# Optimization experiments

Hardware: AMD Instinct MI355X
Metric: run time of the kernel (lower is better)

Reference implementation:

```python
import jax, jax.numpy as jnp
import numpy as np


def _log_kernel(ks, sigma):
    ax = np.arange(-(ks // 2), ks // 2 + 1, dtype=np.float64)
    xx, yy = np.meshgrid(ax, ax, indexing='ij')
    r2 = xx ** 2 + yy ** 2
    gaussian = np.exp(-r2 / (2 * sigma ** 2))
    laplacian = -1.0 / (np.pi * sigma ** 4) * (1.0 - r2 / (2 * sigma ** 2))
    k = laplacian * gaussian
    k = k / np.sum(np.abs(k))
    return jnp.asarray(k, jnp.float32)


def _hpf_kernel(ks):
    if ks == 3:
        k = np.array([[-1, -1, -1], [-1, 8, -1], [-1, -1, -1]], dtype=np.float32)
    else:  # 5
        k = -np.ones((5, 5), dtype=np.float32)
        k[2, 2] = 24.0
    return jnp.asarray(k)


def _lpf_kernel():
    k = np.array([[1, 2, 1], [2, 4, 2], [1, 2, 1]], dtype=np.float32) / 16.0
    return jnp.asarray(k)


def _gabor_kernel(angle, frequency=0.1, sigma_x=2.0, sigma_y=2.0):
    theta = np.radians(angle)
    x, y = np.meshgrid(np.linspace(-3, 3, 7), np.linspace(-3, 3, 7))
    x_t = x * np.cos(theta) + y * np.sin(theta)
    y_t = -x * np.sin(theta) + y * np.cos(theta)
    g = np.exp(-(x_t ** 2 / sigma_x ** 2 + y_t ** 2 / sigma_y ** 2) / 2.0) * np.cos(2 * np.pi * frequency * x_t)
    g = g / np.sum(np.abs(g))
    return jnp.asarray(g, jnp.float32)


def _dwconv(x, k2d, pad):
    # depthwise conv: same single-channel kernel applied to every channel
    C = x.shape[1]
    kern = jnp.broadcast_to(k2d[None, None], (C, 1) + k2d.shape)  # (C,1,kh,kw)
    return jax.lax.conv_general_dilated(
        x, kern, window_strides=(1, 1), padding=[(pad, pad), (pad, pad)],
        feature_group_count=C, dimension_numbers=('NCHW', 'OIHW', 'NCHW'))


def _squash(z):
    # (tanh(z*0.1)+1)/2
    return (jnp.tanh(z * 0.1) + 1.0) * 0.5


def setup_inputs() -> dict:
    key = jax.random.key(0)
    x = jax.random.normal(key, (16, 3, 512, 512), dtype=jnp.float32)
    return {"x": x, "use_gabor": 1}


def reference(x, use_gabor):
    # 'original'
    original = x
    # 'lpf'
    lpf = _dwconv(x, _lpf_kernel(), pad=1)
    # 'log': multi-scale LoG -> squash -> elementwise max over scales
    log3 = _dwconv(x, _log_kernel(3, 0.8), pad=1)
    log5 = _dwconv(x, _log_kernel(5, 1.0), pad=2)
    log7 = _dwconv(x, _log_kernel(7, 1.4), pad=3)
    log_out = jnp.maximum(jnp.maximum(_squash(log3), _squash(log5)), _squash(log7))
    # 'hpf'
    hpf3 = _dwconv(x, _hpf_kernel(3), pad=1)
    hpf5 = _dwconv(x, _hpf_kernel(5), pad=2)
    hpf_out = jnp.maximum(_squash(hpf3), _squash(hpf5))
    outs = (original, lpf, log_out, hpf_out)
    if use_gabor:
        gab = None
        for angle in (0, 45, 90, 135):
            r = jnp.tanh(_dwconv(x, _gabor_kernel(angle), pad=3) * 0.1)
            gab = r if gab is None else jnp.maximum(gab, r)
        outs = outs + (gab,)
    return outs
```

## Files before the change

kernel.cpp:

```cpp
#include <hip/hip_runtime.h>

#define IMG_H 512
#define IMG_W 512
#define TILE_W 64
#define TILE_H 16
#define LDSW 72
#define LDSH 22
#define TCOLS 72
#define TROWS 16
#define NSLOTA (TROWS * (TCOLS / 4))
#define NTHREADS 256


constexpr double PI_D = 3.141592653589793238462643383279502884;

constexpr double cexp(double x) {
  double term = 1.0, sum = 1.0;
  for (int n = 1; n < 48; ++n) { term *= x / n; sum += term; }
  return sum;
}
constexpr double ccos(double x) {
  double term = 1.0, sum = 1.0;
  for (int n = 1; n < 24; ++n) {
    term *= -x * x / ((2.0 * n - 1.0) * (2.0 * n));
    sum += term;
  }
  return sum;
}
constexpr double csin(double x) {
  double term = x, sum = x;
  for (int n = 1; n < 24; ++n) {
    term *= -x * x / ((2.0 * n) * (2.0 * n + 1.0));
    sum += term;
  }
  return sum;
}
constexpr double cabs_(double x) { return x < 0 ? -x : x; }

constexpr void fill_log(int ks, double sigma, float* out) {
  double buf[49] = {};
  double s = 0.0;
  const int h = ks / 2;
  for (int i = 0; i < ks; ++i) {
    for (int j = 0; j < ks; ++j) {
      const double xi = (double)(i - h);
      const double yj = (double)(j - h);
      const double r2 = xi * xi + yj * yj;
      const double g = cexp(-r2 / (2.0 * sigma * sigma));
      const double lap = -1.0 / (PI_D * sigma * sigma * sigma * sigma) *
                         (1.0 - r2 / (2.0 * sigma * sigma));
      buf[i * ks + j] = lap * g;
      s += cabs_(lap * g);
    }
  }
  for (int k = 0; k < ks * ks; ++k) out[k] = (float)(buf[k] / s);
}

constexpr void fill_log_sep(int ks, double sigma, float* va, float* g, float* wb) {
  const int h = ks / 2;
  double s = 0.0;
  for (int i = 0; i < ks; ++i)
    for (int j = 0; j < ks; ++j) {
      const double xi = (double)(i - h), yj = (double)(j - h);
      const double r2 = xi * xi + yj * yj;
      const double gg = cexp(-r2 / (2.0 * sigma * sigma));
      const double lap = -1.0 / (PI_D * sigma * sigma * sigma * sigma) *
                         (1.0 - r2 / (2.0 * sigma * sigma));
      s += cabs_(lap * gg);
    }
  const double c = 1.0 / (PI_D * sigma * sigma * sigma * sigma);
  for (int i = 0; i < ks; ++i) {
    const double d = (double)(i - h);
    const double gi = cexp(-d * d / (2.0 * sigma * sigma));
    g[i] = (float)gi;
    va[i] = (float)((-c + c * d * d / (2.0 * sigma * sigma)) * gi / s);
    wb[i] = (float)((c * d * d / (2.0 * sigma * sigma)) * gi / s);
  }
}

constexpr double gabor_norm(double ang_deg) {
  const double th = ang_deg * PI_D / 180.0;
  const double ct = ccos(th), st = csin(th);
  double s = 0.0;
  for (int i = 0; i < 7; ++i)
    for (int j = 0; j < 7; ++j) {
      const double xv = (double)(j - 3);
      const double yv = (double)(i - 3);
      const double xt = xv * ct + yv * st;
      const double yt = -xv * st + yv * ct;
      const double g = cexp(-(xt * xt / 4.0 + yt * yt / 4.0) / 2.0) *
                       ccos(2.0 * PI_D * 0.1 * xt);
      s += cabs_(g);
    }
  return s;
}

struct SepTabs {
  float l5_va[5], l5_g[5], l5_wb[5];
  float l7_va[7], l7_g[7], l7_wb[7];
  float v_gb[7], v_gc0[7], v_gca[7], v_gsa[7];
  float h_g0[7], h_g90[7], h_gc[7], h_gs[7];
  float is45, is135;
  float l3_m, l3_e, l3_s;
};

constexpr SepTabs make_sep() {
  SepTabs t{};
  fill_log_sep(5, 1.0, t.l5_va, t.l5_g, t.l5_wb);
  fill_log_sep(7, 1.4, t.l7_va, t.l7_g, t.l7_wb);
  const double s0 = gabor_norm(0.0), s90 = gabor_norm(90.0);
  const double s45 = gabor_norm(45.0), s135 = gabor_norm(135.0);
  const double th45 = 45.0 * PI_D / 180.0;
  const double a45 = 2.0 * PI_D * 0.1 * ccos(th45);
  const double b45 = 2.0 * PI_D * 0.1 * csin(th45);
  const double w0 = 2.0 * PI_D * 0.1;
  for (int k = 0; k < 7; ++k) {
    const double d = (double)(k - 3);
    const double gg = cexp(-d * d / 8.0);
    t.v_gb[k]  = (float)gg;
    t.v_gc0[k] = (float)(gg * ccos(w0 * d));
    t.v_gca[k] = (float)(gg * ccos(b45 * d));
    t.v_gsa[k] = (float)(gg * csin(b45 * d));
    t.h_g0[k]  = (float)(gg * ccos(w0 * d) / s0);
    t.h_g90[k] = (float)(gg / s90);
    t.h_gc[k]  = (float)(gg * ccos(a45 * d));
    t.h_gs[k]  = (float)(gg * csin(a45 * d));
  }
  t.is45 = (float)(1.0 / s45);
  t.is135 = (float)(1.0 / s135);
  float l3[9] = {};
  fill_log(3, 0.8, l3);
  t.l3_m = l3[4]; t.l3_e = l3[1]; t.l3_s = l3[0];
  return t;
}

constexpr SepTabs ST = make_sep();


__device__ __forceinline__ float fast_tanh(float x) {
  float e = __builtin_amdgcn_exp2f(x * 2.8853900817779268f);
  return 1.0f - 2.0f * __builtin_amdgcn_rcpf(e + 1.0f);
}
__device__ __forceinline__ float squash_from(float z) {
  return fmaf(fast_tanh(0.1f * z), 0.5f, 0.5f);
}
__device__ __forceinline__ float4 f4z() { return make_float4(0.f, 0.f, 0.f, 0.f); }
__device__ __forceinline__ float4 f4add(float4 a, float4 b) {
  return make_float4(a.x + b.x, a.y + b.y, a.z + b.z, a.w + b.w);
}
__device__ __forceinline__ float4 f4fma(float a, float4 b, float4 c) {
  return make_float4(fmaf(a, b.x, c.x), fmaf(a, b.y, c.y),
                     fmaf(a, b.z, c.z), fmaf(a, b.w, c.w));
}
__device__ __forceinline__ void loadw12(const float* p, float* w) {
  const float4 a = *(const float4*)(p);
  const float4 b = *(const float4*)(p + 4);
  const float4 c = *(const float4*)(p + 8);
  w[0] = a.x; w[1] = a.y; w[2] = a.z; w[3] = a.w;
  w[4] = b.x; w[5] = b.y; w[6] = b.z; w[7] = b.w;
  w[8] = c.x; w[9] = c.y; w[10] = c.z; w[11] = c.w;
}


__global__ __launch_bounds__(NTHREADS, 5)
void msif_kernel(const float* __restrict__ x, float* __restrict__ out,
                 int planes, int do_gab) {
  __shared__ float tile[LDSH * LDSW];
  __shared__ float T[5][TROWS * TCOLS];

  const int tid = threadIdx.x;
  const int tx = tid & 15;
  const int ty = tid >> 4;
  const int x0 = blockIdx.x * TILE_W;
  const int y0 = blockIdx.y * TILE_H;
  const int plane = blockIdx.z;
  const float* __restrict__ in = x + (size_t)plane * (IMG_H * IMG_W);

  const int gx0 = x0 - 4;
  const int gy0 = y0 - 3;
  for (int k = tid; k < LDSH * (LDSW / 4); k += NTHREADS) {
    int r = k / (LDSW / 4);
    int cc = (k - r * (LDSW / 4)) * 4;
    int gy = gy0 + r;
    int gx = gx0 + cc;
    float4 v = make_float4(0.f, 0.f, 0.f, 0.f);
    if ((unsigned)gy < IMG_H) {
      const float* rowp = in + (size_t)gy * IMG_W;
      if (gx >= 0 && gx + 3 < IMG_W) {
        v = *(const float4*)(rowp + gx);
      } else {
        if ((unsigned)(gx + 0) < IMG_W) v.x = rowp[gx + 0];
        if ((unsigned)(gx + 1) < IMG_W) v.y = rowp[gx + 1];
        if ((unsigned)(gx + 2) < IMG_W) v.z = rowp[gx + 2];
        if ((unsigned)(gx + 3) < IMG_W) v.w = rowp[gx + 3];
      }
    }
    *(float4*)&tile[r * LDSW + cc] = v;
  }
  __syncthreads();

  for (int k = tid; k < NSLOTA; k += NTHREADS) {
    const int r = k / (TCOLS / 4);
    const int c4 = (k - r * (TCOLS / 4)) * 4;
    const float* base = &tile[r * LDSW + c4];
    float4 wv[7];
#pragma unroll
    for (int i = 0; i < 7; ++i) wv[i] = *(const float4*)(base + i * LDSW);

    float4 b5 = f4add(f4add(wv[1], wv[2]), f4add(f4add(wv[3], wv[4]), wv[5]));
    float4 l5a = f4z(), l5g = f4z();
#pragma unroll
    for (int i = 0; i < 5; ++i) {
      l5a = f4fma(ST.l5_va[i], wv[i + 1], l5a);
      l5g = f4fma(ST.l5_g[i],  wv[i + 1], l5g);
    }
    float4 l7a = f4z(), l7g = f4z();
#pragma unroll
    for (int i = 0; i < 7; ++i) {
      l7a = f4fma(ST.l7_va[i], wv[i], l7a);
      l7g = f4fma(ST.l7_g[i],  wv[i], l7g);
    }
    const int o = r * TCOLS + c4;
    *(float4*)&T[0][o] = b5;
    *(float4*)&T[1][o] = l5a;
    *(float4*)&T[2][o] = l5g;
    *(float4*)&T[3][o] = l7a;
    *(float4*)&T[4][o] = l7g;
  }
  __syncthreads();

  const size_t fs = (size_t)planes * (IMG_H * IMG_W);
  const size_t off = (size_t)plane * (IMG_H * IMG_W) +
                     (size_t)(y0 + ty) * IMG_W + (x0 + 4 * tx);
  const int toff = ty * TCOLS + 4 * tx;

  {
    float w[12];
    float l7[4] = {}, l5[4] = {}, box[4];

    loadw12(&T[3][toff], w);
#pragma unroll
    for (int dx = 0; dx < 7; ++dx) {
      const float cc = ST.l7_g[dx];
#pragma unroll
      for (int c = 0; c < 4; ++c) l7[c] = fmaf(w[c + dx + 1], cc, l7[c]);
    }
    loadw12(&T[4][toff], w);
#pragma unroll
    for (int dx = 0; dx < 7; ++dx) {
      const float cc = ST.l7_wb[dx];
#pragma unroll
      for (int c = 0; c < 4; ++c) l7[c] = fmaf(w[c + dx + 1], cc, l7[c]);
    }
    loadw12(&T[1][toff], w);
#pragma unroll
    for (int dx = 0; dx < 5; ++dx) {
      const float cc = ST.l5_g[dx];
#pragma unroll
      for (int c = 0; c < 4; ++c) l5[c] = fmaf(w[c + dx + 2], cc, l5[c]);
    }
    loadw12(&T[2][toff], w);
#pragma unroll
    for (int dx = 0; dx < 5; ++dx) {
      const float cc = ST.l5_wb[dx];
#pragma unroll
      for (int c = 0; c < 4; ++c) l5[c] = fmaf(w[c + dx + 2], cc, l5[c]);
    }
    loadw12(&T[0][toff], w);
#pragma unroll
    for (int c = 0; c < 4; ++c)
      box[c] = ((w[c + 2] + w[c + 3]) + (w[c + 4] + w[c + 5])) + w[c + 6];

    float m[4], e[4], s[4];
    loadw12(&tile[(ty + 2) * LDSW + 4 * tx], w);
#pragma unroll
    for (int c = 0; c < 4; ++c) {
      e[c] = w[c + 4];
      s[c] = w[c + 3] + w[c + 5];
    }
    loadw12(&tile[(ty + 4) * LDSW + 4 * tx], w);
#pragma unroll
    for (int c = 0; c < 4; ++c) {
      e[c] += w[c + 4];
      s[c] += w[c + 3] + w[c + 5];
    }
    loadw12(&tile[(ty + 3) * LDSW + 4 * tx], w);
    *(float4*)(out + off) = make_float4(w[4], w[5], w[6], w[7]);
#pragma unroll
    for (int c = 0; c < 4; ++c) {
      m[c] = w[c + 4];
      e[c] += w[c + 3] + w[c + 5];
    }

    float lp[4], lo[4], ho[4];
#pragma unroll
    for (int c = 0; c < 4; ++c) {
      lp[c] = fmaf(0.25f, m[c], fmaf(0.125f, e[c], 0.0625f * s[c]));
      const float l3v = fmaf(ST.l3_m, m[c], fmaf(ST.l3_e, e[c], ST.l3_s * s[c]));
      const float h3v = fmaf(8.f, m[c], -(e[c] + s[c]));
      const float h5v = fmaf(25.f, m[c], -box[c]);
      lo[c] = squash_from(fmaxf(fmaxf(l3v, l5[c]), l7[c]));
      ho[c] = squash_from(fmaxf(h3v, h5v));
    }
    *(float4*)(out + fs + off) = make_float4(lp[0], lp[1], lp[2], lp[3]);
    *(float4*)(out + 2 * fs + off) = make_float4(lo[0], lo[1], lo[2], lo[3]);
    *(float4*)(out + 3 * fs + off) = make_float4(ho[0], ho[1], ho[2], ho[3]);
  }

  if (!do_gab) return;
  __syncthreads();

  for (int k = tid; k < NSLOTA; k += NTHREADS) {
    const int r = k / (TCOLS / 4);
    const int c4 = (k - r * (TCOLS / 4)) * 4;
    const float* base = &tile[r * LDSW + c4];
    float4 gb = f4z(), gc0 = f4z(), gca = f4z(), gsa = f4z();
#pragma unroll
    for (int i = 0; i < 7; ++i) {
      const float4 wv = *(const float4*)(base + i * LDSW);
      gb  = f4fma(ST.v_gb[i],  wv, gb);
      gc0 = f4fma(ST.v_gc0[i], wv, gc0);
      gca = f4fma(ST.v_gca[i], wv, gca);
      gsa = f4fma(ST.v_gsa[i], wv, gsa);
    }
    const int o = r * TCOLS + c4;
    *(float4*)&T[0][o] = gb;
    *(float4*)&T[1][o] = gc0;
    *(float4*)&T[2][o] = gca;
    *(float4*)&T[3][o] = gsa;
  }
  __syncthreads();

  {
    float w[12];
    float g0[4] = {}, g90[4] = {}, Pa[4] = {}, Qa[4] = {};

    loadw12(&T[0][toff], w);
#pragma unroll
    for (int dx = 0; dx < 7; ++dx) {
      const float cc = ST.h_g0[dx];
#pragma unroll
      for (int c = 0; c < 4; ++c) g0[c] = fmaf(w[c + dx + 1], cc, g0[c]);
    }
    loadw12(&T[1][toff], w);
#pragma unroll
    for (int dx = 0; dx < 7; ++dx) {
      const float cc = ST.h_g90[dx];
#pragma unroll
      for (int c = 0; c < 4; ++c) g90[c] = fmaf(w[c + dx + 1], cc, g90[c]);
    }
    loadw12(&T[2][toff], w);
#pragma unroll
    for (int dx = 0; dx < 7; ++dx) {
      const float cc = ST.h_gc[dx];
#pragma unroll
      for (int c = 0; c < 4; ++c) Pa[c] = fmaf(w[c + dx + 1], cc, Pa[c]);
    }
    loadw12(&T[3][toff], w);
#pragma unroll
    for (int dx = 0; dx < 7; ++dx) {
      const float cc = ST.h_gs[dx];
#pragma unroll
      for (int c = 0; c < 4; ++c) Qa[c] = fmaf(w[c + dx + 1], cc, Qa[c]);
    }

    float go[4];
#pragma unroll
    for (int c = 0; c < 4; ++c) {
      const float o45  = (Pa[c] - Qa[c]) * ST.is45;
      const float o135 = (Pa[c] + Qa[c]) * ST.is135;
      go[c] = fast_tanh(0.1f * fmaxf(fmaxf(g0[c], g90[c]), fmaxf(o45, o135)));
    }
    *(float4*)(out + 4 * fs + off) = make_float4(go[0], go[1], go[2], go[3]);
  }
}

extern "C" void kernel_launch(void* const* d_in, const int* in_sizes, int n_in,
                              void* d_out, int out_size, void* d_ws, size_t ws_size,
                              hipStream_t stream) {
  const float* x = (const float*)d_in[0];
  float* out = (float*)d_out;
  const int plane_elems = IMG_H * IMG_W;
  const int planes = in_sizes[0] / plane_elems;
  const int do_gab = (out_size >= 5 * in_sizes[0]) ? 1 : 0;

  dim3 grid(IMG_W / TILE_W, IMG_H / TILE_H, planes);
  msif_kernel<<<grid, NTHREADS, 0, stream>>>(x, out, planes, do_gab);
}
```

Baseline: 312.3 us.

## Drop LDS input tile and read input halo directly from global memory

Removes the shared-memory staging tile and its barrier, so every vertical-pass and 3x3 read pulls float4s straight from global memory (through L1/L2) with per-vector bounds checks. This frees about 6 KB of LDS per block, which allows the launch bound to rise from 5 to 6 blocks per CU. The cost is many more global load instructions, since each input row is reread by several threads and again in the Gabor pass. The whole-vector bounds test assumes the tile edges are 4-aligned, which holds because x0-4 is a multiple of 4.

```diff
diff --git a/kernel.cpp b/kernel.cpp
--- a/kernel.cpp
+++ b/kernel.cpp
@@ -4,8 +4,6 @@
 #define IMG_W 512
 #define TILE_W 64
 #define TILE_H 16
-#define LDSW 72
-#define LDSH 22
 #define TCOLS 72
 #define TROWS 16
 #define NSLOTA (TROWS * (TCOLS / 4))
@@ -160,12 +158,16 @@
   w[4] = b.x; w[5] = b.y; w[6] = b.z; w[7] = b.w;
   w[8] = c.x; w[9] = c.y; w[10] = c.z; w[11] = c.w;
 }
-
-
-__global__ __launch_bounds__(NTHREADS, 5)
+__device__ __forceinline__ float4 gload(const float* __restrict__ p, bool ok) {
+  float4 v = make_float4(0.f, 0.f, 0.f, 0.f);
+  if (ok) v = *(const float4*)p;
+  return v;
+}
+
+
+__global__ __launch_bounds__(NTHREADS, 6)
 void msif_kernel(const float* __restrict__ x, float* __restrict__ out,
                  int planes, int do_gab) {
-  __shared__ float tile[LDSH * LDSW];
   __shared__ float T[5][TROWS * TCOLS];
 
   const int tid = threadIdx.x;
@@ -176,36 +178,19 @@
   const int plane = blockIdx.z;
   const float* __restrict__ in = x + (size_t)plane * (IMG_H * IMG_W);
 
-  const int gx0 = x0 - 4;
-  const int gy0 = y0 - 3;
-  for (int k = tid; k < LDSH * (LDSW / 4); k += NTHREADS) {
-    int r = k / (LDSW / 4);
-    int cc = (k - r * (LDSW / 4)) * 4;
-    int gy = gy0 + r;
-    int gx = gx0 + cc;
-    float4 v = make_float4(0.f, 0.f, 0.f, 0.f);
-    if ((unsigned)gy < IMG_H) {
-      const float* rowp = in + (size_t)gy * IMG_W;
-      if (gx >= 0 && gx + 3 < IMG_W) {
-        v = *(const float4*)(rowp + gx);
-      } else {
-        if ((unsigned)(gx + 0) < IMG_W) v.x = rowp[gx + 0];
-        if ((unsigned)(gx + 1) < IMG_W) v.y = rowp[gx + 1];
-        if ((unsigned)(gx + 2) < IMG_W) v.z = rowp[gx + 2];
-        if ((unsigned)(gx + 3) < IMG_W) v.w = rowp[gx + 3];
-      }
-    }
-    *(float4*)&tile[r * LDSW + cc] = v;
-  }
-  __syncthreads();
-
   for (int k = tid; k < NSLOTA; k += NTHREADS) {
     const int r = k / (TCOLS / 4);
     const int c4 = (k - r * (TCOLS / 4)) * 4;
-    const float* base = &tile[r * LDSW + c4];
+    const int gx = x0 - 4 + c4;
+    const bool xok = (unsigned)gx <= (unsigned)(IMG_W - 4);
+    const int gyb = y0 - 3 + r;
     float4 wv[7];
 #pragma unroll
-    for (int i = 0; i < 7; ++i) wv[i] = *(const float4*)(base + i * LDSW);
+    for (int i = 0; i < 7; ++i) {
+      const int gy = gyb + i;
+      wv[i] = gload(in + (size_t)gy * IMG_W + gx,
+                    xok && (unsigned)gy < IMG_H);
+    }
 
     float4 b5 = f4add(f4add(wv[1], wv[2]), f4add(f4add(wv[3], wv[4]), wv[5]));
     float4 l5a = f4z(), l5g = f4z();
@@ -271,25 +256,55 @@
     for (int c = 0; c < 4; ++c)
       box[c] = ((w[c + 2] + w[c + 3]) + (w[c + 4] + w[c + 5])) + w[c + 6];
 
+    const int gxr = x0 + 4 * tx - 4;
+    const int gyc = y0 + ty;
     float m[4], e[4], s[4];
-    loadw12(&tile[(ty + 2) * LDSW + 4 * tx], w);
-#pragma unroll
-    for (int c = 0; c < 4; ++c) {
-      e[c] = w[c + 4];
-      s[c] = w[c + 3] + w[c + 5];
-    }
-    loadw12(&tile[(ty + 4) * LDSW + 4 * tx], w);
-#pragma unroll
-    for (int c = 0; c < 4; ++c) {
-      e[c] += w[c + 4];
-      s[c] += w[c + 3] + w[c + 5];
-    }
-    loadw12(&tile[(ty + 3) * LDSW + 4 * tx], w);
-    *(float4*)(out + off) = make_float4(w[4], w[5], w[6], w[7]);
-#pragma unroll
-    for (int c = 0; c < 4; ++c) {
-      m[c] = w[c + 4];
-      e[c] += w[c + 3] + w[c + 5];
+    {
+      const int gy = gyc - 1;
+      const bool yok = (unsigned)gy < IMG_H;
+      const float* rp = in + (size_t)gy * IMG_W;
+#pragma unroll
+      for (int j = 0; j < 3; ++j) {
+        const float4 v = gload(rp + gxr + 4 * j,
+                               yok && (unsigned)(gxr + 4 * j) <= (unsigned)(IMG_W - 4));
+        w[4 * j + 0] = v.x; w[4 * j + 1] = v.y; w[4 * j + 2] = v.z; w[4 * j + 3] = v.w;
+      }
+#pragma unroll
+      for (int c = 0; c < 4; ++c) {
+        e[c] = w[c + 4];
+        s[c] = w[c + 3] + w[c + 5];
+      }
+    }
+    {
+      const int gy = gyc + 1;
+      const bool yok = (unsigned)gy < IMG_H;
+      const float* rp = in + (size_t)gy * IMG_W;
+#pragma unroll
+      for (int j = 0; j < 3; ++j) {
+        const float4 v = gload(rp + gxr + 4 * j,
+                               yok && (unsigned)(gxr + 4 * j) <= (unsigned)(IMG_W - 4));
+        w[4 * j + 0] = v.x; w[4 * j + 1] = v.y; w[4 * j + 2] = v.z; w[4 * j + 3] = v.w;
+      }
+#pragma unroll
+      for (int c = 0; c < 4; ++c) {
+        e[c] += w[c + 4];
+        s[c] += w[c + 3] + w[c + 5];
+      }
+    }
+    {
+      const float* rp = in + (size_t)gyc * IMG_W;
+#pragma unroll
+      for (int j = 0; j < 3; ++j) {
+        const float4 v = gload(rp + gxr + 4 * j,
+                               (unsigned)(gxr + 4 * j) <= (unsigned)(IMG_W - 4));
+        w[4 * j + 0] = v.x; w[4 * j + 1] = v.y; w[4 * j + 2] = v.z; w[4 * j + 3] = v.w;
+      }
+      *(float4*)(out + off) = make_float4(w[4], w[5], w[6], w[7]);
+#pragma unroll
+      for (int c = 0; c < 4; ++c) {
+        m[c] = w[c + 4];
+        e[c] += w[c + 3] + w[c + 5];
+      }
     }
 
     float lp[4], lo[4], ho[4];
@@ -313,11 +328,15 @@
   for (int k = tid; k < NSLOTA; k += NTHREADS) {
     const int r = k / (TCOLS / 4);
     const int c4 = (k - r * (TCOLS / 4)) * 4;
-    const float* base = &tile[r * LDSW + c4];
+    const int gx = x0 - 4 + c4;
+    const bool xok = (unsigned)gx <= (unsigned)(IMG_W - 4);
+    const int gyb = y0 - 3 + r;
     float4 gb = f4z(), gc0 = f4z(), gca = f4z(), gsa = f4z();
 #pragma unroll
     for (int i = 0; i < 7; ++i) {
-      const float4 wv = *(const float4*)(base + i * LDSW);
+      const int gy = gyb + i;
+      const float4 wv = gload(in + (size_t)gy * IMG_W + gx,
+                              xok && (unsigned)gy < IMG_H);
       gb  = f4fma(ST.v_gb[i],  wv, gb);
       gc0 = f4fma(ST.v_gc0[i], wv, gc0);
       gca = f4fma(ST.v_gca[i], wv, gca);
```

Result: slower. 340.3 us (+8.9%).
